# Kernel optimization log

Hardware: AMD Instinct MI355X
Metric: run time of the kernel (lower is better)

The kernel has to match this reference:

```python
import jax, jax.numpy as jnp
import numpy as np
import math

IN_C, N_EMBD, HEADS = 256, 512, 8

def setup_inputs() -> dict:
    key = jax.random.key(0)
    ks = jax.random.split(key, 5)
    B, T = 64, 500
    x = jax.random.normal(ks[0], (B, T, IN_C), dtype=jnp.float32)
    # torch Linear: y = x @ W.T + b; store W as [out, in]
    w_attn = jax.random.normal(ks[1], (3 * N_EMBD, IN_C), dtype=jnp.float32) * (1.0 / math.sqrt(IN_C))
    b_attn = jax.random.normal(ks[2], (3 * N_EMBD,), dtype=jnp.float32) * 0.02
    w_proj = jax.random.normal(ks[3], (N_EMBD, N_EMBD), dtype=jnp.float32) * (1.0 / math.sqrt(N_EMBD))
    b_proj = jax.random.normal(ks[4], (N_EMBD,), dtype=jnp.float32) * 0.02
    return {"x": x, "w_attn": w_attn, "b_attn": b_attn, "w_proj": w_proj, "b_proj": b_proj}

def reference(x, w_attn, b_attn, w_proj, b_proj):
    B, T, C = x.shape
    H, D = HEADS, N_EMBD // HEADS
    qkv = jnp.einsum('btc,ec->bte', x, w_attn) + b_attn  # [B,T,3*n_embd]
    q, k, v = jnp.split(qkv, 3, axis=-1)
    # [B,T,n_embd] -> [B,H,T,D]
    q = q.reshape(B, T, H, D).transpose(0, 2, 1, 3)
    k = k.reshape(B, T, H, D).transpose(0, 2, 1, 3)
    v = v.reshape(B, T, H, D).transpose(0, 2, 1, 3)
    att = jnp.einsum('bhtd,bhsd->bhts', q, k) * (1.0 / math.sqrt(D))
    # bias buffer is all-ones: masked_fill(bias==0, -inf) is a no-op
    att = jax.nn.softmax(att, axis=-1)
    y = jnp.einsum('bhts,bhsd->bhtd', att, v)  # [B,H,T,D]
    y = y.transpose(0, 2, 1, 3).reshape(B, T, N_EMBD)
    return jnp.einsum('bte,fe->btf', y, w_proj) + b_proj
```

## Files before the change

### kernel.cpp

```cpp
#include <hip/hip_runtime.h>

typedef _Float16 f16;
typedef _Float16 f16x8 __attribute__((ext_vector_type(8)));
typedef _Float16 f16x4 __attribute__((ext_vector_type(4)));
typedef _Float16 f16x2 __attribute__((ext_vector_type(2)));
typedef float    f32x4 __attribute__((ext_vector_type(4)));
typedef float    f32x16 __attribute__((ext_vector_type(16)));
typedef unsigned int u32;

typedef const __attribute__((address_space(1))) void GVOID;
typedef __attribute__((address_space(3))) void LVOID;

static __device__ __forceinline__ f32x4 mfma16(f16x8 a, f16x8 b, f32x4 c) {
  return __builtin_amdgcn_mfma_f32_16x16x32_f16(a, b, c, 0, 0, 0);
}
static __device__ __forceinline__ f32x16 mfma32(f16x8 a, f16x8 b, f32x16 c) {
  return __builtin_amdgcn_mfma_f32_32x32x16_f16(a, b, c, 0, 0, 0);
}
static __device__ __forceinline__ void gl_lds16(const f16* g, f16* l) {
  __builtin_amdgcn_global_load_lds((GVOID*)g, (LVOID*)l, 16, 0, 0);
}
static __device__ __forceinline__ u32 pk(float a, float b) {
  union { f16x2 h; u32 w; } u;
  u.h[0] = (f16)a; u.h[1] = (f16)b;
  return u.w;
}
static __device__ __forceinline__ u32 pkh(f16 a, f16 b) {
  union { f16x2 h; u32 w; } u;
  u.h[0] = a; u.h[1] = b;
  return u.w;
}
static __device__ __forceinline__ f16x8 mkfrag(float a0, float a1, float a2, float a3,
                                               float a4, float a5, float a6, float a7) {
  u32 c01 = pk(a0, a1), c23 = pk(a2, a3), c45 = pk(a4, a5), c67 = pk(a6, a7);
  asm("v_permlane32_swap_b32 %0, %1" : "+v"(c01), "+v"(c45));
  asm("v_permlane32_swap_b32 %0, %1" : "+v"(c23), "+v"(c67));
  union { f16x8 h; u32 w[4]; } u;
  u.w[0] = c01; u.w[1] = c23; u.w[2] = c45; u.w[3] = c67;
  return u.h;
}

__global__ __launch_bounds__(256)
void cvt_kernel(const float* __restrict__ s, f16* __restrict__ d, int n) {
  int i = (blockIdx.x * 256 + threadIdx.x) * 8;
  if (i >= n) return;
  float4 v0 = *(const float4*)(s + i);
  float4 v1 = *(const float4*)(s + i + 4);
  f16x8 h;
  h[0] = (f16)v0.x; h[1] = (f16)v0.y; h[2] = (f16)v0.z; h[3] = (f16)v0.w;
  h[4] = (f16)v1.x; h[5] = (f16)v1.y; h[6] = (f16)v1.z; h[7] = (f16)v1.w;
  *(f16x8*)(d + i) = h;
}

template<int EPI, int KD, int NDIM>
__global__ __launch_bounds__(256)
void gemm16(const f16* __restrict__ A, const f16* __restrict__ B,
            const float* __restrict__ bias, f16* __restrict__ outH,
            float* __restrict__ outF) {
  constexpr int NB = NDIM / 128;
  const int cpx = gridDim.x >> 3;
  const int id = blockIdx.x;
  const int g = (id & 7) * cpx + (id >> 3);
  const int mb = g / NB, nb = g - mb * NB;
  const int m0 = mb * 128, n0 = nb * 128;

  __shared__ __align__(16) f16 As[128 * 64];
  __shared__ __align__(16) f16 Bs[128 * 64];
  const int tid = threadIdx.x, lane = tid & 63, wid = tid >> 6;
  const int wm = (wid >> 1) * 64, wn = (wid & 1) * 64;
  const int fr = lane & 15, fg = lane >> 4;
  const int e7 = fr & 7;

  f32x4 acc[4][4] = {};

  for (int k0 = 0; k0 < KD; k0 += 64) {
    __syncthreads();
#pragma unroll
    for (int i = 0; i < 4; ++i) {
      int c = i * 256 + tid;
      int row = c >> 3;
      int col = 8 * ((c & 7) ^ (row & 7));
      gl_lds16(A + (size_t)(m0 + row) * KD + k0 + col, &As[c * 8]);
      gl_lds16(B + (size_t)(n0 + row) * KD + k0 + col, &Bs[c * 8]);
    }
    __syncthreads();
#pragma unroll
    for (int kk = 0; kk < 2; ++kk) {
      const int sa = 8 * ((4 * kk + fg) ^ e7);
      f16x8 af[4], bf[4];
#pragma unroll
      for (int t = 0; t < 4; ++t) {
        af[t] = *(const f16x8*)&As[(wm + t * 16 + fr) * 64 + sa];
        bf[t] = *(const f16x8*)&Bs[(wn + t * 16 + fr) * 64 + sa];
      }
#pragma unroll
      for (int mt = 0; mt < 4; ++mt)
#pragma unroll
        for (int nt = 0; nt < 4; ++nt)
          acc[mt][nt] = mfma16(af[mt], bf[nt], acc[mt][nt]);
    }
  }

  float bv[4];
#pragma unroll
  for (int nt = 0; nt < 4; ++nt) bv[nt] = bias[n0 + wn + nt * 16 + fr];
#pragma unroll
  for (int mt = 0; mt < 4; ++mt) {
    int mg = m0 + wm + mt * 16 + fg * 4;
#pragma unroll
    for (int r = 0; r < 4; ++r)
#pragma unroll
      for (int nt = 0; nt < 4; ++nt) {
        int ng = n0 + wn + nt * 16 + fr;
        float v = acc[mt][nt][r] + bv[nt];
        if (EPI == 0) outH[(size_t)(mg + r) * NDIM + ng] = (f16)v;
        else          outF[(size_t)(mg + r) * NDIM + ng] = v;
      }
  }
}

__global__ __launch_bounds__(512, 4)
void attn_kern(const f16* __restrict__ qkv, f16* __restrict__ Yg) {
  __shared__ __align__(16) f16 Kl[2][64 * 64];
  __shared__ __align__(16) f16 VT[2][64 * 64];
  const int id = blockIdx.x;
  const int g = (id & 7) * 128 + (id >> 3);
  const int bh = g >> 1, qt = g & 1;
  const int b = bh >> 3, h = bh & 7;
  const int tid = threadIdx.x, w = tid >> 6;
  const int l31 = tid & 31, hi = (tid & 63) >> 5, e7 = l31 & 7;

  const f16* base  = qkv + (size_t)b * 500 * 1536 + h * 64;
  const f16* Kbase = base + 512;
  const f16* Vbase = base + 1024;

  const int q = qt * 256 + w * 32 + l31;
  const int qc = q < 500 ? q : 499;
  f16x8 qf[4];
  const f16* qp = base + (size_t)qc * 1536 + hi * 8;
#pragma unroll
  for (int ds = 0; ds < 4; ++ds) qf[ds] = *(const f16x8*)(qp + 16 * ds);
  const f16 qs = (f16)(0.125f * 1.44269504f);
#pragma unroll
  for (int ds = 0; ds < 4; ++ds)
#pragma unroll
    for (int j = 0; j < 8; ++j) qf[ds][j] *= qs;

  f32x16 O0 = {}, O1 = {};
  float l = 0.f;

  const int krow = tid >> 3, kcol = 8 * ((tid & 7) ^ (krow & 7));
  const int kvp = (tid & 31) * 2, d4 = (tid >> 5) * 4;
  f16x4 va, vb;
  const f16x4 VZ4 = {};

  {
    gl_lds16(Kbase + (size_t)krow * 1536 + kcol, &Kl[0][tid * 8]);
    const f16* vp0 = Vbase + (size_t)kvp * 1536 + d4;
    va = *(const f16x4*)vp0; vb = *(const f16x4*)(vp0 + 1536);
#pragma unroll
    for (int dd = 0; dd < 4; ++dd) {
      int d = d4 + dd;
      *(u32*)&VT[0][d * 64 + (kvp ^ ((d & 7) << 3))] = pkh(va[dd], vb[dd]);
    }
    __syncthreads();
  }

#pragma unroll 2
  for (int kt = 0; kt < 8; ++kt) {
    const int cur = kt & 1, nxt = cur ^ 1;
    if (kt < 7) {
      const int kvn = (kt + 1) * 64;
      int kr = kvn + krow; kr = kr < 500 ? kr : 499;
      gl_lds16(Kbase + (size_t)kr * 1536 + kcol, &Kl[nxt][tid * 8]);
      int kv = kvn + kvp;
      int kc0 = kv < 500 ? kv : 499, kc1 = kv + 1 < 500 ? kv + 1 : 499;
      va = *(const f16x4*)(Vbase + (size_t)kc0 * 1536 + d4);
      vb = *(const f16x4*)(Vbase + (size_t)kc1 * 1536 + d4);
      if (kv >= 500) va = VZ4;
      if (kv + 1 >= 500) vb = VZ4;
    }

    f32x16 s0 = {}, s1 = {};
    __builtin_amdgcn_s_setprio(1);
#pragma unroll
    for (int ds = 0; ds < 4; ++ds) {
      f16x8 k0 = *(const f16x8*)&Kl[cur][l31 * 64 + 8 * ((hi + 2 * ds) ^ e7)];
      f16x8 k1 = *(const f16x8*)&Kl[cur][(32 + l31) * 64 + 8 * ((hi + 2 * ds) ^ e7)];
      s0 = mfma32(k0, qf[ds], s0);
      s1 = mfma32(k1, qf[ds], s1);
    }
    __builtin_amdgcn_s_setprio(0);

    if (kt == 7) {
#pragma unroll
      for (int r = 0; r < 16; ++r) {
        int kvL = (r & 3) + 8 * (r >> 2) + 4 * hi;
        if (480 + kvL >= 500) s1[r] = -1e30f;
      }
    }

    float ps = 0.f;
#pragma unroll
    for (int r = 0; r < 16; ++r) {
      float t = __builtin_amdgcn_exp2f(s0[r] - 8.f);
      s0[r] = t; ps += t;
    }
#pragma unroll
    for (int r = 0; r < 16; ++r) {
      float t = __builtin_amdgcn_exp2f(s1[r] - 8.f);
      s1[r] = t; ps += t;
    }
    ps += __shfl_xor(ps, 32);
    l += ps;

    f16x8 pf0 = mkfrag(s0[0], s0[1], s0[2], s0[3], s0[4], s0[5], s0[6], s0[7]);
    f16x8 pf1 = mkfrag(s0[8], s0[9], s0[10], s0[11], s0[12], s0[13], s0[14], s0[15]);
    f16x8 pf2 = mkfrag(s1[0], s1[1], s1[2], s1[3], s1[4], s1[5], s1[6], s1[7]);
    f16x8 pf3 = mkfrag(s1[8], s1[9], s1[10], s1[11], s1[12], s1[13], s1[14], s1[15]);

    __builtin_amdgcn_s_setprio(1);
#pragma unroll
    for (int ks = 0; ks < 4; ++ks) {
      f16x8 pf = ks == 0 ? pf0 : ks == 1 ? pf1 : ks == 2 ? pf2 : pf3;
      int sw = (16 * ks + 8 * hi) ^ (e7 << 3);
      f16x8 v0 = *(const f16x8*)&VT[cur][l31 * 64 + sw];
      f16x8 v1 = *(const f16x8*)&VT[cur][(32 + l31) * 64 + sw];
      O0 = mfma32(pf, v0, O0);
      O1 = mfma32(pf, v1, O1);
    }
    __builtin_amdgcn_s_setprio(0);

    if (kt < 7) {
#pragma unroll
      for (int dd = 0; dd < 4; ++dd) {
        int d = d4 + dd;
        *(u32*)&VT[nxt][d * 64 + (kvp ^ ((d & 7) << 3))] = pkh(va[dd], vb[dd]);
      }
    }
    __syncthreads();
  }

  float linv = __builtin_amdgcn_rcpf(l);
#pragma unroll
  for (int r = 0; r < 16; ++r) {
    int rowv = (r & 3) + 8 * (r >> 2) + 4 * hi;
    float li = __shfl(linv, rowv);
    int t = qt * 256 + w * 32 + rowv;
    if (t < 500) {
      size_t rowb = (size_t)(b * 500 + t) * 512 + h * 64;
      Yg[rowb + l31]      = (f16)(O0[r] * li);
      Yg[rowb + 32 + l31] = (f16)(O1[r] * li);
    }
  }
}

extern "C" void kernel_launch(void* const* d_in, const int* in_sizes, int n_in,
                              void* d_out, int out_size, void* d_ws, size_t ws_size,
                              hipStream_t stream) {
  const float* x      = (const float*)d_in[0];
  const float* w_attn = (const float*)d_in[1];
  const float* b_attn = (const float*)d_in[2];
  const float* w_proj = (const float*)d_in[3];
  const float* b_proj = (const float*)d_in[4];
  float* out = (float*)d_out;

  char* wsp = (char*)d_ws;
  f16* Yg   = (f16*)wsp;
  f16* x_h  = (f16*)wsp;
  f16* qkv  = (f16*)(wsp + 32768000);
  f16* wa_h = (f16*)(wsp + 32768000 + 98304000);
  f16* wp_h = (f16*)(wsp + 32768000 + 98304000 + 786432);
  if (ws_size < 132382720) return;

  dim3 blk(256);
  cvt_kernel<<<4000, blk, 0, stream>>>(x, x_h, 8192000);
  cvt_kernel<<<192,  blk, 0, stream>>>(w_attn, wa_h, 393216);
  cvt_kernel<<<128,  blk, 0, stream>>>(w_proj, wp_h, 262144);

  gemm16<0, 256, 1536><<<3000, blk, 0, stream>>>(x_h, wa_h, b_attn, qkv, nullptr);
  attn_kern<<<1024, dim3(512), 0, stream>>>(qkv, Yg);
  gemm16<1, 512, 512><<<1000, blk, 0, stream>>>(Yg, wp_h, b_proj, nullptr, out);
}
```

Baseline: 146.9 us.

## Merge conversion kernels, enlarge GEMM tiles to 256x128 with 32x32 MFMA, drop softmax offset

The three fp32-to-fp16 conversion launches become one kernel that branches on index range. Both GEMMs now use 512-thread blocks with 256x128 tiles, 32x32x16 MFMA instructions, and an XCD mapping that handles grid sizes not divisible by eight. The constant -8 offset before exp2 in the attention softmax is removed. The goal is fewer launches and more data reuse per tile, at the cost of more LDS per block and a possible fp16 overflow in the probabilities once the offset is gone.

```diff
diff --git a/kernel.cpp b/kernel.cpp
--- a/kernel.cpp
+++ b/kernel.cpp
@@ -11,9 +11,6 @@
 typedef const __attribute__((address_space(1))) void GVOID;
 typedef __attribute__((address_space(3))) void LVOID;
 
-static __device__ __forceinline__ f32x4 mfma16(f16x8 a, f16x8 b, f32x4 c) {
-  return __builtin_amdgcn_mfma_f32_16x16x32_f16(a, b, c, 0, 0, 0);
-}
 static __device__ __forceinline__ f32x16 mfma32(f16x8 a, f16x8 b, f32x16 c) {
   return __builtin_amdgcn_mfma_f32_32x32x16_f16(a, b, c, 0, 0, 0);
 }
@@ -41,82 +38,93 @@
 }
 
 __global__ __launch_bounds__(256)
-void cvt_kernel(const float* __restrict__ s, f16* __restrict__ d, int n) {
+void cvt_all(const float* __restrict__ x,  f16* __restrict__ xh,
+             const float* __restrict__ wa, f16* __restrict__ wah,
+             const float* __restrict__ wp, f16* __restrict__ wph) {
   int i = (blockIdx.x * 256 + threadIdx.x) * 8;
-  if (i >= n) return;
-  float4 v0 = *(const float4*)(s + i);
-  float4 v1 = *(const float4*)(s + i + 4);
+  const float* s; f16* d;
+  if (i < 8192000)            { s = x + i;                 d = xh + i; }
+  else if (i < 8192000+393216){ int j = i - 8192000;       s = wa + j; d = wah + j; }
+  else                        { int j = i - 8585216;       s = wp + j; d = wph + j; }
+  float4 v0 = *(const float4*)(s);
+  float4 v1 = *(const float4*)(s + 4);
   f16x8 h;
   h[0] = (f16)v0.x; h[1] = (f16)v0.y; h[2] = (f16)v0.z; h[3] = (f16)v0.w;
   h[4] = (f16)v1.x; h[5] = (f16)v1.y; h[6] = (f16)v1.z; h[7] = (f16)v1.w;
-  *(f16x8*)(d + i) = h;
+  *(f16x8*)d = h;
 }
 
 template<int EPI, int KD, int NDIM>
-__global__ __launch_bounds__(256)
-void gemm16(const f16* __restrict__ A, const f16* __restrict__ B,
-            const float* __restrict__ bias, f16* __restrict__ outH,
-            float* __restrict__ outF) {
+__global__ __launch_bounds__(512)
+void gemm256(const f16* __restrict__ A, const f16* __restrict__ B,
+             const float* __restrict__ bias, f16* __restrict__ outH,
+             float* __restrict__ outF) {
   constexpr int NB = NDIM / 128;
-  const int cpx = gridDim.x >> 3;
-  const int id = blockIdx.x;
-  const int g = (id & 7) * cpx + (id >> 3);
+  const int nwg = gridDim.x;
+  const int orig = blockIdx.x;
+  const int xcd = orig & 7, loc = orig >> 3;
+  const int qq = nwg >> 3, rr8 = nwg & 7;
+  const int g = (xcd < rr8 ? xcd * (qq + 1) : rr8 * (qq + 1) + (xcd - rr8) * qq) + loc;
   const int mb = g / NB, nb = g - mb * NB;
-  const int m0 = mb * 128, n0 = nb * 128;
-
-  __shared__ __align__(16) f16 As[128 * 64];
+  const int m0 = mb * 256, n0 = nb * 128;
+
+  __shared__ __align__(16) f16 As[256 * 64];
   __shared__ __align__(16) f16 Bs[128 * 64];
-  const int tid = threadIdx.x, lane = tid & 63, wid = tid >> 6;
+  const int tid = threadIdx.x, wid = tid >> 6;
+  const int l31 = tid & 31, hi = (tid >> 5) & 1;
   const int wm = (wid >> 1) * 64, wn = (wid & 1) * 64;
-  const int fr = lane & 15, fg = lane >> 4;
-  const int e7 = fr & 7;
-
-  f32x4 acc[4][4] = {};
+
+  f32x16 acc[2][2] = {};
 
   for (int k0 = 0; k0 < KD; k0 += 64) {
     __syncthreads();
 #pragma unroll
     for (int i = 0; i < 4; ++i) {
-      int c = i * 256 + tid;
-      int row = c >> 3;
+      int c = i * 512 + tid, row = c >> 3;
       int col = 8 * ((c & 7) ^ (row & 7));
       gl_lds16(A + (size_t)(m0 + row) * KD + k0 + col, &As[c * 8]);
+    }
+#pragma unroll
+    for (int i = 0; i < 2; ++i) {
+      int c = i * 512 + tid, row = c >> 3;
+      int col = 8 * ((c & 7) ^ (row & 7));
       gl_lds16(B + (size_t)(n0 + row) * KD + k0 + col, &Bs[c * 8]);
     }
     __syncthreads();
 #pragma unroll
-    for (int kk = 0; kk < 2; ++kk) {
-      const int sa = 8 * ((4 * kk + fg) ^ e7);
-      f16x8 af[4], bf[4];
-#pragma unroll
-      for (int t = 0; t < 4; ++t) {
-        af[t] = *(const f16x8*)&As[(wm + t * 16 + fr) * 64 + sa];
-        bf[t] = *(const f16x8*)&Bs[(wn + t * 16 + fr) * 64 + sa];
-      }
-#pragma unroll
-      for (int mt = 0; mt < 4; ++mt)
-#pragma unroll
-        for (int nt = 0; nt < 4; ++nt)
-          acc[mt][nt] = mfma16(af[mt], bf[nt], acc[mt][nt]);
-    }
-  }
-
-  float bv[4];
-#pragma unroll
-  for (int nt = 0; nt < 4; ++nt) bv[nt] = bias[n0 + wn + nt * 16 + fr];
-#pragma unroll
-  for (int mt = 0; mt < 4; ++mt) {
-    int mg = m0 + wm + mt * 16 + fg * 4;
-#pragma unroll
-    for (int r = 0; r < 4; ++r)
-#pragma unroll
-      for (int nt = 0; nt < 4; ++nt) {
-        int ng = n0 + wn + nt * 16 + fr;
-        float v = acc[mt][nt][r] + bv[nt];
-        if (EPI == 0) outH[(size_t)(mg + r) * NDIM + ng] = (f16)v;
-        else          outF[(size_t)(mg + r) * NDIM + ng] = v;
-      }
-  }
+    for (int kk = 0; kk < 4; ++kk) {
+      f16x8 af[2], bf[2];
+#pragma unroll
+      for (int t = 0; t < 2; ++t) {
+        int ra = wm + t * 32 + l31;
+        af[t] = *(const f16x8*)&As[ra * 64 + 8 * ((2 * kk + hi) ^ (ra & 7))];
+        int rb = wn + t * 32 + l31;
+        bf[t] = *(const f16x8*)&Bs[rb * 64 + 8 * ((2 * kk + hi) ^ (rb & 7))];
+      }
+#pragma unroll
+      for (int ms = 0; ms < 2; ++ms)
+#pragma unroll
+        for (int ns = 0; ns < 2; ++ns)
+          acc[ms][ns] = mfma32(af[ms], bf[ns], acc[ms][ns]);
+    }
+  }
+
+  float bv[2];
+  bv[0] = bias[n0 + wn + l31];
+  bv[1] = bias[n0 + wn + 32 + l31];
+#pragma unroll
+  for (int ms = 0; ms < 2; ++ms)
+#pragma unroll
+    for (int ns = 0; ns < 2; ++ns)
+#pragma unroll
+      for (int r = 0; r < 16; ++r) {
+        int mrow = (r & 3) + 8 * (r >> 2) + 4 * hi;
+        int m_g = m0 + wm + ms * 32 + mrow;
+        int n_g = n0 + wn + ns * 32 + l31;
+        float v = acc[ms][ns][r] + bv[ns];
+        if (EPI == 0) outH[(size_t)m_g * NDIM + n_g] = (f16)v;
+        else          outF[(size_t)m_g * NDIM + n_g] = v;
+      }
 }
 
 __global__ __launch_bounds__(512, 4)
@@ -203,12 +211,12 @@
     float ps = 0.f;
 #pragma unroll
     for (int r = 0; r < 16; ++r) {
-      float t = __builtin_amdgcn_exp2f(s0[r] - 8.f);
+      float t = __builtin_amdgcn_exp2f(s0[r]);
       s0[r] = t; ps += t;
     }
 #pragma unroll
     for (int r = 0; r < 16; ++r) {
-      float t = __builtin_amdgcn_exp2f(s1[r] - 8.f);
+      float t = __builtin_amdgcn_exp2f(s1[r]);
       s1[r] = t; ps += t;
     }
     ps += __shfl_xor(ps, 32);
@@ -273,12 +281,9 @@
   f16* wp_h = (f16*)(wsp + 32768000 + 98304000 + 786432);
   if (ws_size < 132382720) return;
 
-  dim3 blk(256);
-  cvt_kernel<<<4000, blk, 0, stream>>>(x, x_h, 8192000);
-  cvt_kernel<<<192,  blk, 0, stream>>>(w_attn, wa_h, 393216);
-  cvt_kernel<<<128,  blk, 0, stream>>>(w_proj, wp_h, 262144);
-
-  gemm16<0, 256, 1536><<<3000, blk, 0, stream>>>(x_h, wa_h, b_attn, qkv, nullptr);
+  cvt_all<<<4320, dim3(256), 0, stream>>>(x, x_h, w_attn, wa_h, w_proj, wp_h);
+
+  gemm256<0, 256, 1536><<<1500, dim3(512), 0, stream>>>(x_h, wa_h, b_attn, qkv, nullptr);
   attn_kern<<<1024, dim3(512), 0, stream>>>(qkv, Yg);
-  gemm16<1, 512, 512><<<1000, blk, 0, stream>>>(Yg, wp_h, b_proj, nullptr, out);
-}
+  gemm256<1, 512, 512><<<500, dim3(512), 0, stream>>>(Yg, wp_h, b_proj, nullptr, out);
+}
```

New measurement: 136.3 us. 7.2% less time.
